# Optimization experiments

Measured on AMD Instinct MI355X. Metric: run time of the kernel, lower is better.

The kernel has to match this reference:

```python
import jax, jax.numpy as jnp
import numpy as np

N = 100_000   # number of local objects (rows of h_local)
E = 800_000   # number of edges (objects of class 'branch')
D = 64        # local hidden dim / out_size
DG = 16       # global hidden dim
FL = 4        # local features per edge
FG = 4        # global features
H = 128       # MLP hidden size


def setup_inputs() -> dict:
    key = jax.random.key(0)
    ks = jax.random.split(key, 20)
    inp = {}
    inp["addr_from"] = jax.random.randint(ks[0], (E,), 0, N)
    inp["addr_to"] = jax.random.randint(ks[1], (E,), 0, N)
    inp["h_local"] = jax.random.normal(ks[2], (N, D), dtype=jnp.float32)
    inp["h_global"] = jax.random.normal(ks[3], (1, DG), dtype=jnp.float32)
    inp["x_local"] = jax.random.normal(ks[4], (E, FL), dtype=jnp.float32)
    inp["x_global"] = jax.random.normal(ks[5], (1, FG), dtype=jnp.float32)
    inp["t"] = jax.random.uniform(ks[6], (1, 1), dtype=jnp.float32)
    din = 2 * D + FL + DG + FG + 1  # concat of [h_from, h_to, x_v, h_g, x_g, t]
    dims = [din, H, H, D]
    i = 7
    for pfx in ("f", "t"):  # one MLP per address field: 'from' and 'to'
        for l in range(3):
            w = (jax.random.normal(ks[i], (dims[l], dims[l + 1])) / np.sqrt(dims[l])).astype(jnp.float32)
            i += 1
            inp[f"{pfx}_W{l}"] = w
            inp[f"{pfx}_b{l}"] = jnp.zeros((dims[l + 1],), jnp.float32)
    return inp


def _mlp(x, W0, b0, W1, b1, W2, b2):
    # MLP: Dense->tanh for each hidden layer, final Dense without activation
    x = jnp.tanh(x @ W0 + b0)
    x = jnp.tanh(x @ W1 + b1)
    return x @ W2 + b2


def reference(addr_from, addr_to, h_local, h_global, x_local, x_global, t,
              f_W0, f_b0, f_W1, f_b1, f_W2, f_b2,
              t_W0, t_b0, t_W1, t_b1, t_W2, t_b2):
    ones = jnp.ones((addr_from.shape[0], 1), h_local.dtype)
    # gather_h_v_local: concat of h_local rows at each address field
    h_v = jnp.concatenate([h_local[addr_from], h_local[addr_to]], axis=1)  # [E, 2D]
    # gather_local_input: [h_v, x_v, h_g*1, x_g*1, t*1], nan_to_num
    inp = jnp.nan_to_num(
        jnp.concatenate([h_v, x_local, h_global * ones, x_global * ones, t * ones], axis=1),
        nan=0,
    )  # [E, 153]
    d_from = jnp.tanh(_mlp(inp, f_W0, f_b0, f_W1, f_b1, f_W2, f_b2))  # [E, D]
    d_to = jnp.tanh(_mlp(inp, t_W0, t_b0, t_W1, t_b1, t_W2, t_b2))    # [E, D]
    delta_sum = (0 * h_local).at[addr_from].add(d_from).at[addr_to].add(d_to)
    return jnp.tanh(delta_sum)
```

## Files before the change

### kernel.cpp

```cpp
#include <hip/hip_runtime.h>
#include <hip/hip_bf16.h>

typedef unsigned int uint;
typedef unsigned short ushort;
typedef _Float16 f16x8 __attribute__((ext_vector_type(8)));
typedef short bf16x8 __attribute__((ext_vector_type(8)));
typedef float f32x4 __attribute__((ext_vector_type(4)));
typedef uint u32x4 __attribute__((ext_vector_type(4)));

#define NE 800000
#define NN 100000
#define TE 64
#define ASTR 168
#define HSTR 136
#define SA 164
#define SH 132

#define F0_OFF 0
#define F1_OFF 20480
#define F2_OFF 36864
#define T0_OFF 45056
#define T1_OFF 65536
#define T2_OFF 81920
#define WPK_TOTAL 90112
#define WPK_BYTES (WPK_TOTAL * 2)

#define MF(a, b, c) __builtin_amdgcn_mfma_f32_16x16x32_f16(a, b, c, 0, 0, 0)

__device__ __forceinline__ float ftanh(float x) {
    float e = __builtin_amdgcn_exp2f(x * 2.885390081777927f);
    return __builtin_fmaf(-2.f, __builtin_amdgcn_rcpf(e + 1.f), 1.f);
}

__device__ __forceinline__ void hsplit(float x, ushort& hi, ushort& lo) {
    _Float16 h = (_Float16)x;
    float r = x - (float)h;
    _Float16 l = (_Float16)r;
    hi = __builtin_bit_cast(ushort, h);
    lo = __builtin_bit_cast(ushort, l);
}

__device__ __forceinline__ void bfsplit(float x, ushort& hi, ushort& lo) {
    uint xb = __builtin_bit_cast(uint, x);
    hi = (ushort)(xb >> 16);
    float hif = __builtin_bit_cast(float, xb & 0xFFFF0000u);
    float res = x - hif;
    lo = (ushort)(__builtin_bit_cast(uint, res) >> 16);
}

__device__ __forceinline__ void split8(const float* v, bf16x8& fh, bf16x8& fl) {
    u32x4 H, L;
#pragma unroll
    for (int i = 0; i < 4; ++i) {
        ushort h0, l0, h1, l1;
        bfsplit(v[2*i],   h0, l0);
        bfsplit(v[2*i+1], h1, l1);
        H[i] = (uint)h0 | ((uint)h1 << 16);
        L[i] = (uint)l0 | ((uint)l1 << 16);
    }
    fh = __builtin_bit_cast(bf16x8, H);
    fl = __builtin_bit_cast(bf16x8, L);
}

__global__ __launch_bounds__(256) void pack_w(
    const float* __restrict__ fW0, const float* __restrict__ fW1, const float* __restrict__ fW2,
    const float* __restrict__ tW0, const float* __restrict__ tW1, const float* __restrict__ tW2,
    ushort* __restrict__ wpk)
{
    int idx = blockIdx.x * 256 + threadIdx.x;
    const float* src; int NP, KC, Kact, base;
    if      (idx < F1_OFF) { src = fW0; NP = 4; KC = 5; Kact = 153; base = F0_OFF; }
    else if (idx < F2_OFF) { src = fW1; NP = 4; KC = 4; Kact = 128; base = F1_OFF; }
    else if (idx < T0_OFF) { src = fW2; NP = 2; KC = 4; Kact = 128; base = F2_OFF; }
    else if (idx < T1_OFF) { src = tW0; NP = 4; KC = 5; Kact = 153; base = T0_OFF; }
    else if (idx < T2_OFF) { src = tW1; NP = 4; KC = 4; Kact = 128; base = T1_OFF; }
    else                   { src = tW2; NP = 2; KC = 4; Kact = 128; base = T2_OFF; }
    int rel  = idx - base;
    int j    = rel & 7;
    int lane = (rel >> 3) & 63;
    int sub  = rel >> 9;
    int i    = sub & 1;
    int s2   = sub >> 1;
    int kc   = s2 % KC;
    int np   = s2 / KC;
    int k = kc * 32 + ((lane >> 4) << 3) + j;
    int n = np * 32 + i * 16 + (lane & 15);
    int N = NP * 32;
    float w = (k < Kact) ? src[(size_t)k * N + n] : 0.f;
    _Float16 h = (_Float16)w;
    wpk[idx] = __builtin_bit_cast(ushort, h);
}

template<int KC>
__device__ __forceinline__ void kloop1(const ushort* __restrict__ ap, int astr,
                                       const ushort* __restrict__ gWl,
                                       f32x4 (&acc)[2][2])
{
#pragma unroll
    for (int kc = 0; kc < KC; ++kc) {
        f16x8 a0 = *(const f16x8*)(ap + kc * 32);
        f16x8 a1 = *(const f16x8*)(ap + 16 * astr + kc * 32);
        f16x8 w0 = *(const f16x8*)(gWl + kc * 1024);
        f16x8 w1 = *(const f16x8*)(gWl + kc * 1024 + 512);
        acc[0][0] = MF(a0, w0, acc[0][0]);
        acc[1][0] = MF(a1, w0, acc[1][0]);
        acc[0][1] = MF(a0, w1, acc[0][1]);
        acc[1][1] = MF(a1, w1, acc[1][1]);
    }
}

__device__ __forceinline__ void acc_init(f32x4 (&acc)[2][2],
                                         const float* __restrict__ bias,
                                         int npv, int nn)
{
#pragma unroll
    for (int ni = 0; ni < 2; ++ni) {
        float bv = bias[npv * 32 + ni * 16 + nn];
#pragma unroll
        for (int mi = 0; mi < 2; ++mi)
#pragma unroll
            for (int r = 0; r < 4; ++r) acc[mi][ni][r] = bv;
    }
}

__device__ __forceinline__ void epi_store(const f32x4 (&acc)[2][2],
                                          ushort* __restrict__ sO, int ostr,
                                          int mt, int nn, int kq, int npv)
{
#pragma unroll
    for (int mi = 0; mi < 2; ++mi)
#pragma unroll
        for (int ni = 0; ni < 2; ++ni) {
            int n = npv * 32 + ni * 16 + nn;
#pragma unroll
            for (int r = 0; r < 4; ++r) {
                int m = mt * 32 + mi * 16 + kq * 4 + r;
                _Float16 hh = (_Float16)ftanh(acc[mi][ni][r]);
                sO[m * ostr + n] = __builtin_bit_cast(ushort, hh);
            }
        }
}

__global__ __launch_bounds__(512, 4) void edge_mlp_packed(
    const int* __restrict__ af_, const int* __restrict__ at_,
    const float* __restrict__ h_local, const float* __restrict__ h_global,
    const float* __restrict__ x_local, const float* __restrict__ x_global,
    const float* __restrict__ tsc,
    const float* __restrict__ fb0, const float* __restrict__ fb1, const float* __restrict__ fb2,
    const float* __restrict__ tb0, const float* __restrict__ tb1, const float* __restrict__ tb2,
    const ushort* __restrict__ wpk, float* __restrict__ out)
{
    __shared__ ushort sAh[TE * ASTR], sAl[TE * ASTR];
    __shared__ ushort sHf[TE * HSTR], sHt[TE * HSTR];
    __shared__ int s_af[TE], s_at[TE];

    const int tid = threadIdx.x;
    const int e = tid >> 3, part = tid & 7;
    const int eg = blockIdx.x * TE + e;
    {
        int af = af_[eg], at = at_[eg];
        if (part == 0) { s_af[e] = af; s_at[e] = at; }
        int node = (part < 4) ? af : at;
        int k0 = ((part & 3) << 4) + ((part < 4) ? 0 : 64);
        const float4* hp = (const float4*)(h_local + (size_t)node * 64 + ((part & 3) << 4));
        float4 q0 = hp[0], q1 = hp[1], q2 = hp[2], q3 = hp[3];
        float v[16] = {q0.x,q0.y,q0.z,q0.w, q1.x,q1.y,q1.z,q1.w,
                       q2.x,q2.y,q2.z,q2.w, q3.x,q3.y,q3.z,q3.w};
        u32x4 H0, H1, L0, L1;
#pragma unroll
        for (int i = 0; i < 4; ++i) {
            ushort h0, l0, h1, l1;
            hsplit(v[2*i], h0, l0); hsplit(v[2*i+1], h1, l1);
            H0[i] = (uint)h0 | ((uint)h1 << 16);
            L0[i] = (uint)l0 | ((uint)l1 << 16);
        }
#pragma unroll
        for (int i = 0; i < 4; ++i) {
            ushort h0, l0, h1, l1;
            hsplit(v[8+2*i], h0, l0); hsplit(v[8+2*i+1], h1, l1);
            H1[i] = (uint)h0 | ((uint)h1 << 16);
            L1[i] = (uint)l0 | ((uint)l1 << 16);
        }
        *(u32x4*)(sAh + e * ASTR + k0)     = H0;
        *(u32x4*)(sAh + e * ASTR + k0 + 8) = H1;
        *(u32x4*)(sAl + e * ASTR + k0)     = L0;
        *(u32x4*)(sAl + e * ASTR + k0 + 8) = L1;
        if (part < 2) {
            int k0t = 128 + part * 16;
            float w[16];
#pragma unroll
            for (int i = 0; i < 16; ++i) {
                int k = k0t + i;
                float x;
                if      (k < 132)  x = x_local[(size_t)eg * 4 + (k - 128)];
                else if (k < 148)  x = h_global[k - 132];
                else if (k < 152)  x = x_global[k - 148];
                else if (k == 152) x = tsc[0];
                else               x = 0.f;
                w[i] = x;
            }
            u32x4 H2, H3, L2, L3;
#pragma unroll
            for (int i = 0; i < 4; ++i) {
                ushort h0, l0, h1, l1;
                hsplit(w[2*i], h0, l0); hsplit(w[2*i+1], h1, l1);
                H2[i] = (uint)h0 | ((uint)h1 << 16);
                L2[i] = (uint)l0 | ((uint)l1 << 16);
            }
#pragma unroll
            for (int i = 0; i < 4; ++i) {
                ushort h0, l0, h1, l1;
                hsplit(w[8+2*i], h0, l0); hsplit(w[8+2*i+1], h1, l1);
                H3[i] = (uint)h0 | ((uint)h1 << 16);
                L3[i] = (uint)l0 | ((uint)l1 << 16);
            }
            *(u32x4*)(sAh + e * ASTR + k0t)     = H2;
            *(u32x4*)(sAh + e * ASTR + k0t + 8) = H3;
            *(u32x4*)(sAl + e * ASTR + k0t)     = L2;
            *(u32x4*)(sAl + e * ASTR + k0t + 8) = L3;
        }
    }
    __syncthreads();

    const int lane = tid & 63;
    const int wave = tid >> 6;
    const int mt   = wave >> 2;
    const int np   = wave & 3;
    const int nn   = lane & 15;
    const int kq   = (lane >> 4) & 3;
    const int npu  = __builtin_amdgcn_readfirstlane(np);

    {
        f32x4 af[2][2], at2[2][2];
        acc_init(af,  fb0, np, nn);
        acc_init(at2, tb0, np, nn);
        const ushort* apH = sAh + (mt * 32 + nn) * ASTR + kq * 8;
        const ushort* apL = sAl + (mt * 32 + nn) * ASTR + kq * 8;
        const ushort* gF = wpk + F0_OFF + npu * (5 * 1024) + lane * 8;
        const ushort* gT = wpk + T0_OFF + npu * (5 * 1024) + lane * 8;
#pragma unroll
        for (int kc = 0; kc < 5; ++kc) {
            f16x8 a0 = *(const f16x8*)(apH + kc * 32);
            f16x8 a1 = *(const f16x8*)(apH + 16 * ASTR + kc * 32);
            f16x8 l0 = *(const f16x8*)(apL + kc * 32);
            f16x8 l1 = *(const f16x8*)(apL + 16 * ASTR + kc * 32);
            f16x8 w0 = *(const f16x8*)(gF + kc * 1024);
            f16x8 w1 = *(const f16x8*)(gF + kc * 1024 + 512);
            f16x8 u0 = *(const f16x8*)(gT + kc * 1024);
            f16x8 u1 = *(const f16x8*)(gT + kc * 1024 + 512);
            af[0][0]  = MF(a0, w0, af[0][0]);  af[1][0]  = MF(a1, w0, af[1][0]);
            af[0][1]  = MF(a0, w1, af[0][1]);  af[1][1]  = MF(a1, w1, af[1][1]);
            at2[0][0] = MF(a0, u0, at2[0][0]); at2[1][0] = MF(a1, u0, at2[1][0]);
            at2[0][1] = MF(a0, u1, at2[0][1]); at2[1][1] = MF(a1, u1, at2[1][1]);
            af[0][0]  = MF(l0, w0, af[0][0]);  af[1][0]  = MF(l1, w0, af[1][0]);
            af[0][1]  = MF(l0, w1, af[0][1]);  af[1][1]  = MF(l1, w1, af[1][1]);
            at2[0][0] = MF(l0, u0, at2[0][0]); at2[1][0] = MF(l1, u0, at2[1][0]);
            at2[0][1] = MF(l0, u1, at2[0][1]); at2[1][1] = MF(l1, u1, at2[1][1]);
        }
        epi_store(af,  sHf, HSTR, mt, nn, kq, np);
        epi_store(at2, sHt, HSTR, mt, nn, kq, np);
    }
    __syncthreads();

    {
        f32x4 af[2][2], at2[2][2];
        acc_init(af,  fb1, np, nn);
        acc_init(at2, tb1, np, nn);
        const ushort* apf = sHf + (mt * 32 + nn) * HSTR + kq * 8;
        const ushort* apt = sHt + (mt * 32 + nn) * HSTR + kq * 8;
        kloop1<4>(apf, HSTR, wpk + F1_OFF + npu * 4096 + lane * 8, af);
        kloop1<4>(apt, HSTR, wpk + T1_OFF + npu * 4096 + lane * 8, at2);
        __syncthreads();
        epi_store(af,  sHf, HSTR, mt, nn, kq, np);
        epi_store(at2, sHt, HSTR, mt, nn, kq, np);
    }
    __syncthreads();

    {
        const int sel  = __builtin_amdgcn_readfirstlane(np >> 1);
        const int np2  = __builtin_amdgcn_readfirstlane(np & 1);
        const ushort* sH  = sel ? sHt : sHf;
        const ushort* gW2 = wpk + (sel ? T2_OFF : F2_OFF) + np2 * 4096 + lane * 8;
        const float* b2   = sel ? tb2 : fb2;
        const int* nds    = sel ? s_at : s_af;

        f32x4 acc[2][2];
        acc_init(acc, b2, np2, nn);
        const ushort* ap = sH + (mt * 32 + nn) * HSTR + kq * 8;
        kloop1<4>(ap, HSTR, gW2, acc);
#pragma unroll
        for (int mi = 0; mi < 2; ++mi)
#pragma unroll
            for (int ni = 0; ni < 2; ++ni) {
                int n = np2 * 32 + ni * 16 + nn;
#pragma unroll
                for (int r = 0; r < 4; ++r) {
                    int m = mt * 32 + mi * 16 + kq * 4 + r;
                    float h = ftanh(acc[mi][ni][r]);
                    unsafeAtomicAdd(out + (size_t)nds[m] * 64 + n, h);
                }
            }
    }
}

template<int KC, int NT, int KACT, bool SCATTER>
__device__ __forceinline__ void layer(
    const float* __restrict__ sA, int astr,
    const float* __restrict__ gW, const float* __restrict__ bias,
    float* __restrict__ sO,
    float* __restrict__ out, const int* __restrict__ s_nodes, int tid)
{
    constexpr int NTW = NT / 2;
    constexpr int N = NT * 16;
    const int lane = tid & 63;
    const int wave = tid >> 6;
    const int mt   = wave >> 1;
    const int ntb  = (wave & 1) * NTW;
    const int arow = mt * 16 + (lane & 15);
    const int kg   = (lane >> 4) * 8;
    const int nn   = lane & 15;

    f32x4 aHH[NTW], aLH[NTW], aHL[NTW];
#pragma unroll
    for (int i = 0; i < NTW; ++i)
#pragma unroll
        for (int r = 0; r < 4; ++r) { aHH[i][r] = 0.f; aLH[i][r] = 0.f; aHL[i][r] = 0.f; }

#pragma unroll
    for (int kc = 0; kc < KC; ++kc) {
        const float* ap = sA + arow * astr + kc * 32 + kg;
        float av[8];
        float4 a0 = *(const float4*)ap;
        float4 a1 = *(const float4*)(ap + 4);
        av[0]=a0.x; av[1]=a0.y; av[2]=a0.z; av[3]=a0.w;
        av[4]=a1.x; av[5]=a1.y; av[6]=a1.z; av[7]=a1.w;
        bf16x8 ah, al; split8(av, ah, al);
#pragma unroll
        for (int i = 0; i < NTW; ++i) {
            int n = (ntb + i) * 16 + nn;
            float wv[8];
#pragma unroll
            for (int j = 0; j < 8; ++j) {
                int k = kc * 32 + kg + j;
                float w = 0.f;
                if (KC * 32 <= KACT || k < KACT)
                    w = gW[(size_t)k * N + n];
                wv[j] = w;
            }
            bf16x8 bh, bl; split8(wv, bh, bl);
            aHH[i] = __builtin_amdgcn_mfma_f32_16x16x32_bf16(ah, bh, aHH[i], 0, 0, 0);
            aLH[i] = __builtin_amdgcn_mfma_f32_16x16x32_bf16(al, bh, aLH[i], 0, 0, 0);
            aHL[i] = __builtin_amdgcn_mfma_f32_16x16x32_bf16(ah, bl, aHL[i], 0, 0, 0);
        }
    }

    if (!SCATTER) __syncthreads();

#pragma unroll
    for (int i = 0; i < NTW; ++i) {
        int n = (ntb + i) * 16 + nn;
        float bv = bias[n];
#pragma unroll
        for (int r = 0; r < 4; ++r) {
            int m = mt * 16 + ((lane >> 4) << 2) + r;
            float h = ftanh(aHH[i][r] + aLH[i][r] + aHL[i][r] + bv);
            if (SCATTER) {
                unsafeAtomicAdd(out + (size_t)s_nodes[m] * 64 + n, h);
            } else {
                sO[m * SH + n] = h;
            }
        }
    }
}

__global__ __launch_bounds__(512) void edge_mlp_gather(
    const int* __restrict__ af_, const int* __restrict__ at_,
    const float* __restrict__ h_local, const float* __restrict__ h_global,
    const float* __restrict__ x_local, const float* __restrict__ x_global,
    const float* __restrict__ tsc,
    const float* __restrict__ fW0, const float* __restrict__ fb0,
    const float* __restrict__ fW1, const float* __restrict__ fb1,
    const float* __restrict__ fW2, const float* __restrict__ fb2,
    const float* __restrict__ tW0, const float* __restrict__ tb0,
    const float* __restrict__ tW1, const float* __restrict__ tb1,
    const float* __restrict__ tW2, const float* __restrict__ tb2,
    float* __restrict__ out)
{
    __shared__ float sA[TE * SA];
    __shared__ float sH[TE * SH];
    __shared__ int s_af[TE], s_at[TE];

    const int tid = threadIdx.x;
    const int e = tid >> 3, part = tid & 7;
    const int eg = blockIdx.x * TE + e;
    {
        int af = af_[eg], at = at_[eg];
        if (part == 0) { s_af[e] = af; s_at[e] = at; }
        int node = (part < 4) ? af : at;
        int k0 = ((part & 3) << 4) + ((part < 4) ? 0 : 64);
        const float4* hp = (const float4*)(h_local + (size_t)node * 64 + ((part & 3) << 4));
        float4* dst = (float4*)(sA + e * SA + k0);
        dst[0] = hp[0]; dst[1] = hp[1]; dst[2] = hp[2]; dst[3] = hp[3];
        if (part < 2) {
            int k0t = 128 + part * 16;
#pragma unroll
            for (int i = 0; i < 16; ++i) {
                int k = k0t + i;
                float x;
                if      (k < 132)  x = x_local[(size_t)eg * 4 + (k - 128)];
                else if (k < 148)  x = h_global[k - 132];
                else if (k < 152)  x = x_global[k - 148];
                else if (k == 152) x = tsc[0];
                else               x = 0.f;
                sA[e * SA + k] = x;
            }
        }
    }
    __syncthreads();
    layer<5,8,153,false>(sA, SA, fW0, fb0, sH, nullptr, nullptr, tid);
    __syncthreads();
    layer<4,8,128,false>(sH, SH, fW1, fb1, sH, nullptr, nullptr, tid);
    __syncthreads();
    layer<4,4,128,true >(sH, SH, fW2, fb2, nullptr, out, s_af, tid);
    __syncthreads();
    layer<5,8,153,false>(sA, SA, tW0, tb0, sH, nullptr, nullptr, tid);
    __syncthreads();
    layer<4,8,128,false>(sH, SH, tW1, tb1, sH, nullptr, nullptr, tid);
    __syncthreads();
    layer<4,4,128,true >(sH, SH, tW2, tb2, nullptr, out, s_at, tid);
}

__global__ __launch_bounds__(256) void tanh_kernel(float* __restrict__ out, int n4) {
    int i = blockIdx.x * blockDim.x + threadIdx.x;
    int stride = gridDim.x * blockDim.x;
    float4* p = (float4*)out;
    for (; i < n4; i += stride) {
        float4 v = p[i];
        v.x = ftanh(v.x); v.y = ftanh(v.y); v.z = ftanh(v.z); v.w = ftanh(v.w);
        p[i] = v;
    }
}

extern "C" void kernel_launch(void* const* d_in, const int* in_sizes, int n_in,
                              void* d_out, int out_size, void* d_ws, size_t ws_size,
                              hipStream_t stream) {
    const int*   addr_from = (const int*)d_in[0];
    const int*   addr_to   = (const int*)d_in[1];
    const float* h_local   = (const float*)d_in[2];
    const float* h_global  = (const float*)d_in[3];
    const float* x_local   = (const float*)d_in[4];
    const float* x_global  = (const float*)d_in[5];
    const float* tsc       = (const float*)d_in[6];
    const float* fW0 = (const float*)d_in[7];
    const float* fb0 = (const float*)d_in[8];
    const float* fW1 = (const float*)d_in[9];
    const float* fb1 = (const float*)d_in[10];
    const float* fW2 = (const float*)d_in[11];
    const float* fb2 = (const float*)d_in[12];
    const float* tW0 = (const float*)d_in[13];
    const float* tb0 = (const float*)d_in[14];
    const float* tW1 = (const float*)d_in[15];
    const float* tb1 = (const float*)d_in[16];
    const float* tW2 = (const float*)d_in[17];
    const float* tb2 = (const float*)d_in[18];
    float* out = (float*)d_out;

    hipMemsetAsync(d_out, 0, (size_t)NN * 64 * sizeof(float), stream);

    if (ws_size >= (size_t)WPK_BYTES) {
        ushort* wpk = (ushort*)d_ws;
        pack_w<<<WPK_TOTAL / 256, 256, 0, stream>>>(fW0, fW1, fW2, tW0, tW1, tW2, wpk);
        edge_mlp_packed<<<NE / TE, 512, 0, stream>>>(
            addr_from, addr_to, h_local, h_global, x_local, x_global, tsc,
            fb0, fb1, fb2, tb0, tb1, tb2, wpk, out);
    } else {
        edge_mlp_gather<<<NE / TE, 512, 0, stream>>>(
            addr_from, addr_to, h_local, h_global, x_local, x_global, tsc,
            fW0, fb0, fW1, fb1, fW2, fb2, tW0, tb0, tW1, tb1, tW2, tb2, out);
    }
    tanh_kernel<<<2048, 256, 0, stream>>>(out, NN * 64 / 4);
}
```

Measured before the change: 416.1 us.

## Drop fp16 hi/lo split of layer-0 input and alias shared buffers for occupancy

Removes the two-term fp16 split of the gathered layer-0 inputs, keeping only the high half. This halves the layer-0 MFMA count and the shared staging. The 'to' hidden buffer now aliases the input buffer, with an extra barrier, and the layer-0 stride is trimmed, cutting LDS per block enough to raise launch bounds to 8 blocks per CU. The cost is lower precision of the first-layer inputs, since h_local values are now rounded to single fp16, plus one added synchronisation.

```diff
diff --git a/kernel.cpp b/kernel.cpp
--- a/kernel.cpp
+++ b/kernel.cpp
@@ -11,7 +11,7 @@
 #define NE 800000
 #define NN 100000
 #define TE 64
-#define ASTR 168
+#define ASTR 160
 #define HSTR 136
 #define SA 164
 #define SH 132
@@ -32,12 +32,10 @@
     return __builtin_fmaf(-2.f, __builtin_amdgcn_rcpf(e + 1.f), 1.f);
 }
 
-__device__ __forceinline__ void hsplit(float x, ushort& hi, ushort& lo) {
-    _Float16 h = (_Float16)x;
-    float r = x - (float)h;
-    _Float16 l = (_Float16)r;
-    hi = __builtin_bit_cast(ushort, h);
-    lo = __builtin_bit_cast(ushort, l);
+__device__ __forceinline__ uint pkh(float a, float b) {
+    _Float16 ha = (_Float16)a, hb = (_Float16)b;
+    return (uint)__builtin_bit_cast(ushort, ha) |
+           ((uint)__builtin_bit_cast(ushort, hb) << 16);
 }
 
 __device__ __forceinline__ void bfsplit(float x, ushort& hi, ushort& lo) {
@@ -141,7 +139,7 @@
         }
 }
 
-__global__ __launch_bounds__(512, 4) void edge_mlp_packed(
+__global__ __launch_bounds__(512, 8) void edge_mlp_packed(
     const int* __restrict__ af_, const int* __restrict__ at_,
     const float* __restrict__ h_local, const float* __restrict__ h_global,
     const float* __restrict__ x_local, const float* __restrict__ x_global,
@@ -150,9 +148,10 @@
     const float* __restrict__ tb0, const float* __restrict__ tb1, const float* __restrict__ tb2,
     const ushort* __restrict__ wpk, float* __restrict__ out)
 {
-    __shared__ ushort sAh[TE * ASTR], sAl[TE * ASTR];
-    __shared__ ushort sHf[TE * HSTR], sHt[TE * HSTR];
+    __shared__ ushort sAh[TE * ASTR];
+    __shared__ ushort sHf[TE * HSTR];
     __shared__ int s_af[TE], s_at[TE];
+    ushort* sAt = sAh;
 
     const int tid = threadIdx.x;
     const int e = tid >> 3, part = tid & 7;
@@ -164,27 +163,13 @@
         int k0 = ((part & 3) << 4) + ((part < 4) ? 0 : 64);
         const float4* hp = (const float4*)(h_local + (size_t)node * 64 + ((part & 3) << 4));
         float4 q0 = hp[0], q1 = hp[1], q2 = hp[2], q3 = hp[3];
-        float v[16] = {q0.x,q0.y,q0.z,q0.w, q1.x,q1.y,q1.z,q1.w,
-                       q2.x,q2.y,q2.z,q2.w, q3.x,q3.y,q3.z,q3.w};
-        u32x4 H0, H1, L0, L1;
-#pragma unroll
-        for (int i = 0; i < 4; ++i) {
-            ushort h0, l0, h1, l1;
-            hsplit(v[2*i], h0, l0); hsplit(v[2*i+1], h1, l1);
-            H0[i] = (uint)h0 | ((uint)h1 << 16);
-            L0[i] = (uint)l0 | ((uint)l1 << 16);
-        }
-#pragma unroll
-        for (int i = 0; i < 4; ++i) {
-            ushort h0, l0, h1, l1;
-            hsplit(v[8+2*i], h0, l0); hsplit(v[8+2*i+1], h1, l1);
-            H1[i] = (uint)h0 | ((uint)h1 << 16);
-            L1[i] = (uint)l0 | ((uint)l1 << 16);
-        }
+        u32x4 H0, H1;
+        H0[0] = pkh(q0.x, q0.y); H0[1] = pkh(q0.z, q0.w);
+        H0[2] = pkh(q1.x, q1.y); H0[3] = pkh(q1.z, q1.w);
+        H1[0] = pkh(q2.x, q2.y); H1[1] = pkh(q2.z, q2.w);
+        H1[2] = pkh(q3.x, q3.y); H1[3] = pkh(q3.z, q3.w);
         *(u32x4*)(sAh + e * ASTR + k0)     = H0;
         *(u32x4*)(sAh + e * ASTR + k0 + 8) = H1;
-        *(u32x4*)(sAl + e * ASTR + k0)     = L0;
-        *(u32x4*)(sAl + e * ASTR + k0 + 8) = L1;
         if (part < 2) {
             int k0t = 128 + part * 16;
             float w[16];
@@ -199,25 +184,13 @@
                 else               x = 0.f;
                 w[i] = x;
             }
-            u32x4 H2, H3, L2, L3;
-#pragma unroll
-            for (int i = 0; i < 4; ++i) {
-                ushort h0, l0, h1, l1;
-                hsplit(w[2*i], h0, l0); hsplit(w[2*i+1], h1, l1);
-                H2[i] = (uint)h0 | ((uint)h1 << 16);
-                L2[i] = (uint)l0 | ((uint)l1 << 16);
-            }
-#pragma unroll
-            for (int i = 0; i < 4; ++i) {
-                ushort h0, l0, h1, l1;
-                hsplit(w[8+2*i], h0, l0); hsplit(w[8+2*i+1], h1, l1);
-                H3[i] = (uint)h0 | ((uint)h1 << 16);
-                L3[i] = (uint)l0 | ((uint)l1 << 16);
-            }
+            u32x4 H2, H3;
+#pragma unroll
+            for (int i = 0; i < 4; ++i) H2[i] = pkh(w[2*i], w[2*i+1]);
+#pragma unroll
+            for (int i = 0; i < 4; ++i) H3[i] = pkh(w[8+2*i], w[8+2*i+1]);
             *(u32x4*)(sAh + e * ASTR + k0t)     = H2;
             *(u32x4*)(sAh + e * ASTR + k0t + 8) = H3;
-            *(u32x4*)(sAl + e * ASTR + k0t)     = L2;
-            *(u32x4*)(sAl + e * ASTR + k0t + 8) = L3;
         }
     }
     __syncthreads();
@@ -234,16 +207,13 @@
         f32x4 af[2][2], at2[2][2];
         acc_init(af,  fb0, np, nn);
         acc_init(at2, tb0, np, nn);
-        const ushort* apH = sAh + (mt * 32 + nn) * ASTR + kq * 8;
-        const ushort* apL = sAl + (mt * 32 + nn) * ASTR + kq * 8;
+        const ushort* ap = sAh + (mt * 32 + nn) * ASTR + kq * 8;
         const ushort* gF = wpk + F0_OFF + npu * (5 * 1024) + lane * 8;
         const ushort* gT = wpk + T0_OFF + npu * (5 * 1024) + lane * 8;
 #pragma unroll
         for (int kc = 0; kc < 5; ++kc) {
-            f16x8 a0 = *(const f16x8*)(apH + kc * 32);
-            f16x8 a1 = *(const f16x8*)(apH + 16 * ASTR + kc * 32);
-            f16x8 l0 = *(const f16x8*)(apL + kc * 32);
-            f16x8 l1 = *(const f16x8*)(apL + 16 * ASTR + kc * 32);
+            f16x8 a0 = *(const f16x8*)(ap + kc * 32);
+            f16x8 a1 = *(const f16x8*)(ap + 16 * ASTR + kc * 32);
             f16x8 w0 = *(const f16x8*)(gF + kc * 1024);
             f16x8 w1 = *(const f16x8*)(gF + kc * 1024 + 512);
             f16x8 u0 = *(const f16x8*)(gT + kc * 1024);
@@ -252,13 +222,10 @@
             af[0][1]  = MF(a0, w1, af[0][1]);  af[1][1]  = MF(a1, w1, af[1][1]);
             at2[0][0] = MF(a0, u0, at2[0][0]); at2[1][0] = MF(a1, u0, at2[1][0]);
             at2[0][1] = MF(a0, u1, at2[0][1]); at2[1][1] = MF(a1, u1, at2[1][1]);
-            af[0][0]  = MF(l0, w0, af[0][0]);  af[1][0]  = MF(l1, w0, af[1][0]);
-            af[0][1]  = MF(l0, w1, af[0][1]);  af[1][1]  = MF(l1, w1, af[1][1]);
-            at2[0][0] = MF(l0, u0, at2[0][0]); at2[1][0] = MF(l1, u0, at2[1][0]);
-            at2[0][1] = MF(l0, u1, at2[0][1]); at2[1][1] = MF(l1, u1, at2[1][1]);
-        }
-        epi_store(af,  sHf, HSTR, mt, nn, kq, np);
-        epi_store(at2, sHt, HSTR, mt, nn, kq, np);
+        }
+        epi_store(af, sHf, HSTR, mt, nn, kq, np);
+        __syncthreads();
+        epi_store(at2, sAt, HSTR, mt, nn, kq, np);
     }
     __syncthreads();
 
@@ -267,19 +234,19 @@
         acc_init(af,  fb1, np, nn);
         acc_init(at2, tb1, np, nn);
         const ushort* apf = sHf + (mt * 32 + nn) * HSTR + kq * 8;
-        const ushort* apt = sHt + (mt * 32 + nn) * HSTR + kq * 8;
+        const ushort* apt = sAt + (mt * 32 + nn) * HSTR + kq * 8;
         kloop1<4>(apf, HSTR, wpk + F1_OFF + npu * 4096 + lane * 8, af);
         kloop1<4>(apt, HSTR, wpk + T1_OFF + npu * 4096 + lane * 8, at2);
         __syncthreads();
         epi_store(af,  sHf, HSTR, mt, nn, kq, np);
-        epi_store(at2, sHt, HSTR, mt, nn, kq, np);
+        epi_store(at2, sAt, HSTR, mt, nn, kq, np);
     }
     __syncthreads();
 
     {
-        const int sel  = __builtin_amdgcn_readfirstlane(np >> 1);
-        const int np2  = __builtin_amdgcn_readfirstlane(np & 1);
-        const ushort* sH  = sel ? sHt : sHf;
+        const int sel = __builtin_amdgcn_readfirstlane(np >> 1);
+        const int np2 = __builtin_amdgcn_readfirstlane(np & 1);
+        const ushort* sH  = sel ? sAt : sHf;
         const ushort* gW2 = wpk + (sel ? T2_OFF : F2_OFF) + np2 * 4096 + lane * 8;
         const float* b2   = sel ? tb2 : fb2;
         const int* nds    = sel ? s_at : s_af;
```

Result: no change. 422.2 us (+1.5%).
